# Optimization experiments

Hardware: AMD Instinct MI355X
Metric: run time of the kernel (lower is better)

Reference implementation:

```python
import jax, jax.numpy as jnp
import numpy as np

BATCH = 2048
INPUT_SIZE = 2048
OUTPUT_SIZE = 2048
N_INPUTS = 6            # fan-in per LUT node
K = 1 << N_INPUTS       # 64 table entries per node


def setup_inputs() -> dict:
    key = jax.random.key(0)
    k1, k2, k3 = jax.random.split(key, 3)
    x = jax.random.uniform(k1, (BATCH, INPUT_SIZE), dtype=jnp.float32)
    table = jax.random.normal(k2, (OUTPUT_SIZE, K), dtype=jnp.float32)
    mapping = jax.random.randint(k3, (OUTPUT_SIZE, N_INPUTS), 0, INPUT_SIZE, dtype=jnp.int64)
    return {"x": x, "table": table, "mapping": mapping}


def reference(x, table, mapping):
    # x: (B, I) in [0,1]; table: (O, 2^n) raw logits; mapping: (O, n) int indices
    O, n = mapping.shape
    Kv = 1 << n
    # per-node input gather -> (B, O, n)
    xg = x[:, mapping]
    # binary codes of the 2^n LUT vertices: bits[k, i] = i-th bit of k
    bits = ((jnp.arange(Kv)[:, None] >> jnp.arange(n)[None, :]) & 1).astype(x.dtype)  # (K, n)
    # vertex probabilities prod_i (x_i if bit else 1-x_i), built by a tiny fixed loop over n
    probs = jnp.ones((x.shape[0], O, Kv), dtype=x.dtype)
    for i in range(n):
        xi = xg[:, :, i][:, :, None]                      # (B, O, 1)
        bi = bits[:, i][None, None, :]                    # (1, 1, K)
        probs = probs * (xi * bi + (1.0 - xi) * (1.0 - bi))
    # differentiable LUT lookup: expected table value under vertex distribution
    out = jnp.einsum('bok,ok->bo', probs, jax.nn.sigmoid(table))  # (B, O)
    return out
```

## Files before the change

kernel.cpp:

```cpp
#include <hip/hip_runtime.h>
#include <math.h>

#define B_TOTAL 2048
#define I_TOTAL 2048
#define O_TOTAL 2048
#define KW 64
#define NIN 6
#define BLOCK 256
#define TILE_B 16
#define CH 4
#define BBLOCKS (B_TOTAL / TILE_B)
#define OBLOCKS (O_TOTAL / BLOCK)

__global__ void prep_kernel(const float* __restrict__ table,
                            const unsigned int* __restrict__ map_raw,
                            float* __restrict__ wT,
                            int* __restrict__ m32T)
{
    int idx = blockIdx.x * blockDim.x + threadIdx.x;
    int o = idx >> 6, k = idx & 63;
    float s = 1.0f / (1.0f + __expf(-table[idx]));
    float v;
    if (k >= 32) {
        float s0 = 1.0f / (1.0f + __expf(-table[idx - 32]));
        v = s - s0;
    } else {
        v = s;
    }
    wT[k * O_TOTAL + o] = v;

    if (idx < O_TOTAL * NIN) {
        bool is64 = ((map_raw[1] | map_raw[3] | map_raw[5] | map_raw[7]) == 0u);
        int val = is64 ? (int)map_raw[2 * idx] : (int)map_raw[idx];
        int oo = idx / NIN, ii = idx - oo * NIN;
        m32T[ii * O_TOTAL + oo] = val;
    }
}

__global__ __launch_bounds__(BLOCK) void lut_main(
    const float* __restrict__ x,
    const float* __restrict__ wT,
    const int*   __restrict__ m32T,
    float*       __restrict__ out)
{
    __shared__ float xs[CH * I_TOTAL];

    const int o  = blockIdx.y * BLOCK + threadIdx.x;
    const int b0 = blockIdx.x * TILE_B;

    float ww[KW];
    #pragma unroll
    for (int k = 0; k < KW; ++k) ww[k] = wT[k * O_TOTAL + o];

    int m[NIN];
    #pragma unroll
    for (int i = 0; i < NIN; ++i) m[i] = m32T[i * O_TOTAL + o];

    #pragma unroll
    for (int c = 0; c < TILE_B / CH; ++c) {
        __syncthreads();
        const float4* src = (const float4*)(x + (size_t)(b0 + c * CH) * I_TOTAL);
        float4* dst = (float4*)xs;
        #pragma unroll
        for (int t = 0; t < (CH * I_TOTAL / 4) / BLOCK; ++t)
            dst[t * BLOCK + threadIdx.x] = src[t * BLOCK + threadIdx.x];
        __syncthreads();

        #pragma unroll
        for (int cr = 0; cr < CH; ++cr) {
            const float* xr = xs + cr * I_TOTAL;
            float xv[NIN];
            #pragma unroll
            for (int i = 0; i < NIN; ++i) xv[i] = xr[m[i]];

            float t[32];
            #pragma unroll
            for (int j = 0; j < 32; ++j) t[j] = fmaf(xv[5], ww[j + 32], ww[j]);
            #pragma unroll
            for (int j = 0; j < 16; ++j) t[j] = fmaf(xv[4], t[j + 16] - t[j], t[j]);
            #pragma unroll
            for (int j = 0; j < 8;  ++j) t[j] = fmaf(xv[3], t[j + 8]  - t[j], t[j]);
            #pragma unroll
            for (int j = 0; j < 4;  ++j) t[j] = fmaf(xv[2], t[j + 4]  - t[j], t[j]);
            #pragma unroll
            for (int j = 0; j < 2;  ++j) t[j] = fmaf(xv[1], t[j + 2]  - t[j], t[j]);
            float res = fmaf(xv[0], t[1] - t[0], t[0]);

            out[(size_t)(b0 + c * CH + cr) * O_TOTAL + o] = res;
        }
    }
}

extern "C" void kernel_launch(void* const* d_in, const int* in_sizes, int n_in,
                              void* d_out, int out_size, void* d_ws, size_t ws_size,
                              hipStream_t stream)
{
    const float*        x       = (const float*)d_in[0];
    const float*        table   = (const float*)d_in[1];
    const unsigned int* map_raw = (const unsigned int*)d_in[2];
    float* out  = (float*)d_out;
    float* wT   = (float*)d_ws;
    int*   m32T = (int*)((char*)d_ws + (size_t)O_TOTAL * KW * sizeof(float));

    prep_kernel<<<(O_TOTAL * KW) / BLOCK, BLOCK, 0, stream>>>(table, map_raw, wT, m32T);

    dim3 grid(BBLOCKS, OBLOCKS);
    lut_main<<<grid, dim3(BLOCK), 0, stream>>>(x, wT, m32T, out);
}
```

Measured before the change: 85.81 us.

## Double-buffer x tiles with async global-to-LDS loads and transpose prep via LDS

The main kernel now double-buffers the x row chunks in LDS and uses global_load_lds async copies, so the next chunk is prefetched while the current one is computed. The chunk size is halved so the two buffers fit, and launch bounds request 3 blocks per CU. The prep kernel is rewritten to transpose the sigmoid table through shared memory, which gives coalesced writes, and it runs on 48 blocks. The risks are correctness of the async LDS copy (the offset and lane layout must match what the builtin expects) and extra register pressure from the occupancy hint.

```diff
diff --git a/kernel.cpp b/kernel.cpp
--- a/kernel.cpp
+++ b/kernel.cpp
@@ -8,45 +8,69 @@
 #define NIN 6
 #define BLOCK 256
 #define TILE_B 16
-#define CH 4
+#define CH 2
+#define NCHUNK (TILE_B / CH)
 #define BBLOCKS (B_TOTAL / TILE_B)
 #define OBLOCKS (O_TOTAL / BLOCK)
 
-__global__ void prep_kernel(const float* __restrict__ table,
-                            const unsigned int* __restrict__ map_raw,
-                            float* __restrict__ wT,
-                            int* __restrict__ m32T)
+__global__ __launch_bounds__(BLOCK) void prep_kernel(
+    const float* __restrict__ table,
+    const unsigned int* __restrict__ map_raw,
+    float* __restrict__ wT,
+    int* __restrict__ m32T)
 {
-    int idx = blockIdx.x * blockDim.x + threadIdx.x;
-    int o = idx >> 6, k = idx & 63;
-    float s = 1.0f / (1.0f + __expf(-table[idx]));
-    float v;
-    if (k >= 32) {
-        float s0 = 1.0f / (1.0f + __expf(-table[idx - 32]));
-        v = s - s0;
-    } else {
-        v = s;
+    const int t = threadIdx.x;
+
+    if (blockIdx.x < 32) {
+        __shared__ float sm[64][65];
+        const int o0 = blockIdx.x * 64;
+        #pragma unroll
+        for (int rep = 0; rep < 16; ++rep) {
+            int idx = rep * 256 + t;
+            int ol = idx >> 6, k = idx & 63;
+            float v = table[(o0 + ol) * KW + k];
+            sm[ol][k] = 1.0f / (1.0f + __expf(-v));
+        }
+        __syncthreads();
+        #pragma unroll
+        for (int rep = 0; rep < 16; ++rep) {
+            int idx = rep * 256 + t;
+            int k = idx >> 6, ol = idx & 63;
+            float s = sm[ol][k];
+            float v = (k >= 32) ? (s - sm[ol][k - 32]) : s;
+            wT[k * O_TOTAL + o0 + ol] = v;
+        }
     }
-    wT[k * O_TOTAL + o] = v;
 
-    if (idx < O_TOTAL * NIN) {
+    const int gid = blockIdx.x * BLOCK + t;
+    if (gid < O_TOTAL * NIN) {
         bool is64 = ((map_raw[1] | map_raw[3] | map_raw[5] | map_raw[7]) == 0u);
-        int val = is64 ? (int)map_raw[2 * idx] : (int)map_raw[idx];
-        int oo = idx / NIN, ii = idx - oo * NIN;
+        int val = is64 ? (int)map_raw[2 * gid] : (int)map_raw[gid];
+        int oo = gid / NIN, ii = gid - oo * NIN;
         m32T[ii * O_TOTAL + oo] = val;
     }
 }
 
-__global__ __launch_bounds__(BLOCK) void lut_main(
+__device__ __forceinline__ void async_cp16(float* lds, const float* g)
+{
+    __builtin_amdgcn_global_load_lds(
+        (const __attribute__((address_space(1))) void*)g,
+        (__attribute__((address_space(3))) void*)lds,
+        16, 0, 0);
+}
+
+__global__ __launch_bounds__(BLOCK, 3) void lut_main(
     const float* __restrict__ x,
     const float* __restrict__ wT,
     const int*   __restrict__ m32T,
     float*       __restrict__ out)
 {
-    __shared__ float xs[CH * I_TOTAL];
+    __shared__ float xs[2 * CH * I_TOTAL];
 
-    const int o  = blockIdx.y * BLOCK + threadIdx.x;
-    const int b0 = blockIdx.x * TILE_B;
+    const int o    = blockIdx.y * BLOCK + threadIdx.x;
+    const int b0   = blockIdx.x * TILE_B;
+    const int wave = threadIdx.x >> 6;
+    const int lane = threadIdx.x & 63;
 
     float ww[KW];
     #pragma unroll
@@ -56,38 +80,54 @@
     #pragma unroll
     for (int i = 0; i < NIN; ++i) m[i] = m32T[i * O_TOTAL + o];
 
-    #pragma unroll
-    for (int c = 0; c < TILE_B / CH; ++c) {
-        __syncthreads();
-        const float4* src = (const float4*)(x + (size_t)(b0 + c * CH) * I_TOTAL);
-        float4* dst = (float4*)xs;
+    {
+        const float* src = x + (size_t)b0 * I_TOTAL;
         #pragma unroll
-        for (int t = 0; t < (CH * I_TOTAL / 4) / BLOCK; ++t)
-            dst[t * BLOCK + threadIdx.x] = src[t * BLOCK + threadIdx.x];
-        __syncthreads();
+        for (int ti = 0; ti < 4; ++ti) {
+            int off = (wave * 4 + ti) * 256;
+            async_cp16(&xs[off], src + off + lane * 4);
+        }
+    }
+    __syncthreads();
+
+    #pragma unroll 2
+    for (int c = 0; c < NCHUNK; ++c) {
+        const int buf = c & 1;
+
+        if (c + 1 < NCHUNK) {
+            const float* src = x + (size_t)(b0 + (c + 1) * CH) * I_TOTAL;
+            float* dst = &xs[(buf ^ 1) * CH * I_TOTAL];
+            #pragma unroll
+            for (int ti = 0; ti < 4; ++ti) {
+                int off = (wave * 4 + ti) * 256;
+                async_cp16(dst + off, src + off + lane * 4);
+            }
+        }
 
         #pragma unroll
         for (int cr = 0; cr < CH; ++cr) {
-            const float* xr = xs + cr * I_TOTAL;
+            const int rowc = (buf * CH + cr) * I_TOTAL;
             float xv[NIN];
             #pragma unroll
-            for (int i = 0; i < NIN; ++i) xv[i] = xr[m[i]];
+            for (int i = 0; i < NIN; ++i) xv[i] = xs[rowc + m[i]];
 
-            float t[32];
+            float tt[32];
             #pragma unroll
-            for (int j = 0; j < 32; ++j) t[j] = fmaf(xv[5], ww[j + 32], ww[j]);
+            for (int j = 0; j < 32; ++j) tt[j] = fmaf(xv[5], ww[j + 32], ww[j]);
             #pragma unroll
-            for (int j = 0; j < 16; ++j) t[j] = fmaf(xv[4], t[j + 16] - t[j], t[j]);
+            for (int j = 0; j < 16; ++j) tt[j] = fmaf(xv[4], tt[j + 16] - tt[j], tt[j]);
             #pragma unroll
-            for (int j = 0; j < 8;  ++j) t[j] = fmaf(xv[3], t[j + 8]  - t[j], t[j]);
+            for (int j = 0; j < 8;  ++j) tt[j] = fmaf(xv[3], tt[j + 8]  - tt[j], tt[j]);
             #pragma unroll
-            for (int j = 0; j < 4;  ++j) t[j] = fmaf(xv[2], t[j + 4]  - t[j], t[j]);
+            for (int j = 0; j < 4;  ++j) tt[j] = fmaf(xv[2], tt[j + 4]  - tt[j], tt[j]);
             #pragma unroll
-            for (int j = 0; j < 2;  ++j) t[j] = fmaf(xv[1], t[j + 2]  - t[j], t[j]);
-            float res = fmaf(xv[0], t[1] - t[0], t[0]);
+            for (int j = 0; j < 2;  ++j) tt[j] = fmaf(xv[1], tt[j + 2]  - tt[j], tt[j]);
+            float res = fmaf(xv[0], tt[1] - tt[0], tt[0]);
 
             out[(size_t)(b0 + c * CH + cr) * O_TOTAL + o] = res;
         }
+
+        __syncthreads();
     }
 }
 
@@ -102,7 +142,7 @@
     float* wT   = (float*)d_ws;
     int*   m32T = (int*)((char*)d_ws + (size_t)O_TOTAL * KW * sizeof(float));
 
-    prep_kernel<<<(O_TOTAL * KW) / BLOCK, BLOCK, 0, stream>>>(table, map_raw, wT, m32T);
+    prep_kernel<<<48, BLOCK, 0, stream>>>(table, map_raw, wT, m32T);
 
     dim3 grid(BBLOCKS, OBLOCKS);
     lut_main<<<grid, dim3(BLOCK), 0, stream>>>(x, wT, m32T, out);
```

Result: no change. 85.28 us (median of 2 runs) (-0.6%).

## Transpose x to input-major layout and map threads to batch rows

Applied to the files above, without the earlier changes.

Adds a tiled shared-memory transpose of x so that each input column is contiguous over the batch, then remaps the main kernel so threads cover batch rows and each block loops over 16 outputs with uniform (broadcast) table and mapping loads. Output tiles are staged in shared memory so stores to the output are coalesced. This replaces the per-block 32KB staging of x rows plus scattered LDS gathers with coalesced global gathers. The cost is an extra full 16MB read and write pass over x in the prep kernel, plus the larger workspace it needs.

```diff
diff --git a/kernel.cpp b/kernel.cpp
--- a/kernel.cpp
+++ b/kernel.cpp
@@ -7,87 +7,111 @@
 #define KW 64
 #define NIN 6
 #define BLOCK 256
-#define TILE_B 16
-#define CH 4
-#define BBLOCKS (B_TOTAL / TILE_B)
-#define OBLOCKS (O_TOTAL / BLOCK)
+#define T_O 16
+#define TPOSE_BLOCKS 1024
+#define WPREP_BLOCKS 512
+#define MAIN_BLOCKS ((B_TOTAL / BLOCK) * (O_TOTAL / T_O))
 
-__global__ void prep_kernel(const float* __restrict__ table,
-                            const unsigned int* __restrict__ map_raw,
-                            float* __restrict__ wT,
-                            int* __restrict__ m32T)
+__global__ __launch_bounds__(BLOCK) void prep_all(
+    const float* __restrict__ x,
+    const float* __restrict__ table,
+    const unsigned int* __restrict__ map_raw,
+    float* __restrict__ xT,
+    float* __restrict__ wP,
+    int*   __restrict__ m32)
 {
-    int idx = blockIdx.x * blockDim.x + threadIdx.x;
-    int o = idx >> 6, k = idx & 63;
-    float s = 1.0f / (1.0f + __expf(-table[idx]));
-    float v;
-    if (k >= 32) {
-        float s0 = 1.0f / (1.0f + __expf(-table[idx - 32]));
-        v = s - s0;
+    const int bid = blockIdx.x, tid = threadIdx.x;
+
+    if (bid < TPOSE_BLOCKS) {
+        __shared__ float sm[64][65];
+        const int bi = bid >> 5, bj = bid & 31;
+        const int col = tid & 63, w = tid >> 6;
+        #pragma unroll
+        for (int r8 = 0; r8 < 16; ++r8) {
+            int row = r8 * 4 + w;
+            sm[row][col] = x[(size_t)(bi * 64 + row) * I_TOTAL + bj * 64 + col];
+        }
+        __syncthreads();
+        #pragma unroll
+        for (int r8 = 0; r8 < 16; ++r8) {
+            int row = r8 * 4 + w;
+            xT[(size_t)(bj * 64 + row) * B_TOTAL + bi * 64 + col] = sm[col][row];
+        }
     } else {
-        v = s;
-    }
-    wT[k * O_TOTAL + o] = v;
+        const int gid = (bid - TPOSE_BLOCKS) * BLOCK + tid;
+        float v = table[gid];
+        float s = 1.0f / (1.0f + __expf(-v));
+        if ((gid & 63) >= 32) {
+            float v0 = table[gid - 32];
+            s -= 1.0f / (1.0f + __expf(-v0));
+        }
+        wP[gid] = s;
 
-    if (idx < O_TOTAL * NIN) {
-        bool is64 = ((map_raw[1] | map_raw[3] | map_raw[5] | map_raw[7]) == 0u);
-        int val = is64 ? (int)map_raw[2 * idx] : (int)map_raw[idx];
-        int oo = idx / NIN, ii = idx - oo * NIN;
-        m32T[ii * O_TOTAL + oo] = val;
+        if (gid < O_TOTAL * NIN) {
+            bool is64 = ((map_raw[1] | map_raw[3] | map_raw[5] | map_raw[7]) == 0u);
+            m32[gid] = is64 ? (int)map_raw[2 * gid] : (int)map_raw[gid];
+        }
     }
 }
 
-__global__ __launch_bounds__(BLOCK) void lut_main(
-    const float* __restrict__ x,
-    const float* __restrict__ wT,
-    const int*   __restrict__ m32T,
+__global__ __launch_bounds__(BLOCK, 2) void lut_main(
+    const float* __restrict__ xT,
+    const float* __restrict__ wP,
+    const int*   __restrict__ m32,
     float*       __restrict__ out)
 {
-    __shared__ float xs[CH * I_TOTAL];
+    __shared__ float os[T_O][BLOCK + 2];
 
-    const int o  = blockIdx.y * BLOCK + threadIdx.x;
-    const int b0 = blockIdx.x * TILE_B;
+    const int tid = threadIdx.x, bid = blockIdx.x;
+    const int bx = bid & 7;
+    const int oy = bid >> 3;
+    const int o0 = oy * T_O;
+    const float* xb = xT + (size_t)bx * BLOCK + tid;
 
-    float ww[KW];
-    #pragma unroll
-    for (int k = 0; k < KW; ++k) ww[k] = wT[k * O_TOTAL + o];
+    #pragma unroll 2
+    for (int ol = 0; ol < T_O; ++ol) {
+        const int o = o0 + ol;
 
-    int m[NIN];
-    #pragma unroll
-    for (int i = 0; i < NIN; ++i) m[i] = m32T[i * O_TOTAL + o];
+        const int* mp = m32 + o * NIN;
+        float xv[NIN];
+        #pragma unroll
+        for (int i = 0; i < NIN; ++i)
+            xv[i] = xb[(size_t)mp[i] * B_TOTAL];
+
+        const float4* wp = (const float4*)(wP + (size_t)o * KW);
+        float4 wa[16];
+        #pragma unroll
+        for (int j = 0; j < 16; ++j) wa[j] = wp[j];
+
+        float tt[32];
+        #pragma unroll
+        for (int j = 0; j < 8; ++j) {
+            tt[4 * j + 0] = fmaf(xv[5], wa[j + 8].x, wa[j].x);
+            tt[4 * j + 1] = fmaf(xv[5], wa[j + 8].y, wa[j].y);
+            tt[4 * j + 2] = fmaf(xv[5], wa[j + 8].z, wa[j].z);
+            tt[4 * j + 3] = fmaf(xv[5], wa[j + 8].w, wa[j].w);
+        }
+        #pragma unroll
+        for (int j = 0; j < 16; ++j) tt[j] = fmaf(xv[4], tt[j + 16] - tt[j], tt[j]);
+        #pragma unroll
+        for (int j = 0; j < 8;  ++j) tt[j] = fmaf(xv[3], tt[j + 8]  - tt[j], tt[j]);
+        #pragma unroll
+        for (int j = 0; j < 4;  ++j) tt[j] = fmaf(xv[2], tt[j + 4]  - tt[j], tt[j]);
+        #pragma unroll
+        for (int j = 0; j < 2;  ++j) tt[j] = fmaf(xv[1], tt[j + 2]  - tt[j], tt[j]);
+        float res = fmaf(xv[0], tt[1] - tt[0], tt[0]);
+
+        os[ol][tid] = res;
+    }
+
+    __syncthreads();
 
     #pragma unroll
-    for (int c = 0; c < TILE_B / CH; ++c) {
-        __syncthreads();
-        const float4* src = (const float4*)(x + (size_t)(b0 + c * CH) * I_TOTAL);
-        float4* dst = (float4*)xs;
-        #pragma unroll
-        for (int t = 0; t < (CH * I_TOTAL / 4) / BLOCK; ++t)
-            dst[t * BLOCK + threadIdx.x] = src[t * BLOCK + threadIdx.x];
-        __syncthreads();
-
-        #pragma unroll
-        for (int cr = 0; cr < CH; ++cr) {
-            const float* xr = xs + cr * I_TOTAL;
-            float xv[NIN];
-            #pragma unroll
-            for (int i = 0; i < NIN; ++i) xv[i] = xr[m[i]];
-
-            float t[32];
-            #pragma unroll
-            for (int j = 0; j < 32; ++j) t[j] = fmaf(xv[5], ww[j + 32], ww[j]);
-            #pragma unroll
-            for (int j = 0; j < 16; ++j) t[j] = fmaf(xv[4], t[j + 16] - t[j], t[j]);
-            #pragma unroll
-            for (int j = 0; j < 8;  ++j) t[j] = fmaf(xv[3], t[j + 8]  - t[j], t[j]);
-            #pragma unroll
-            for (int j = 0; j < 4;  ++j) t[j] = fmaf(xv[2], t[j + 4]  - t[j], t[j]);
-            #pragma unroll
-            for (int j = 0; j < 2;  ++j) t[j] = fmaf(xv[1], t[j + 2]  - t[j], t[j]);
-            float res = fmaf(xv[0], t[1] - t[0], t[0]);
-
-            out[(size_t)(b0 + c * CH + cr) * O_TOTAL + o] = res;
-        }
+    for (int rep = 0; rep < T_O; ++rep) {
+        int idx = rep * BLOCK + tid;
+        int o_l = idx & (T_O - 1);
+        int r   = idx / T_O;
+        out[(size_t)(bx * BLOCK + r) * O_TOTAL + o0 + o_l] = os[o_l][r];
     }
 }
 
@@ -98,12 +122,14 @@
     const float*        x       = (const float*)d_in[0];
     const float*        table   = (const float*)d_in[1];
     const unsigned int* map_raw = (const unsigned int*)d_in[2];
-    float* out  = (float*)d_out;
-    float* wT   = (float*)d_ws;
-    int*   m32T = (int*)((char*)d_ws + (size_t)O_TOTAL * KW * sizeof(float));
+    float* out = (float*)d_out;
 
-    prep_kernel<<<(O_TOTAL * KW) / BLOCK, BLOCK, 0, stream>>>(table, map_raw, wT, m32T);
+    float* xT  = (float*)d_ws;
+    float* wP  = (float*)((char*)d_ws + (size_t)16 * 1024 * 1024);
+    int*   m32 = (int*)  ((char*)d_ws + (size_t)16 * 1024 * 1024 + 512 * 1024);
 
-    dim3 grid(BBLOCKS, OBLOCKS);
-    lut_main<<<grid, dim3(BLOCK), 0, stream>>>(x, wT, m32T, out);
+    prep_all<<<TPOSE_BLOCKS + WPREP_BLOCKS, BLOCK, 0, stream>>>(
+        x, table, map_raw, xT, wP, m32);
+
+    lut_main<<<MAIN_BLOCKS, BLOCK, 0, stream>>>(xT, wP, m32, out);
 }
```

Result: slower. 96.16 us (+12.1%).
